# Performance work log

Measured on AMD Instinct MI355X. Metric: run time of the kernel, lower is better.

The kernel has to match this reference:

```python
import math
import jax, jax.numpy as jnp
import numpy as np

D_MODEL = 1024
N_HEADS = 8
D_CONV = 4
D_INNER = 2 * D_MODEL
D_HIDDEN = 2 * D_MODEL
DH = D_INNER // N_HEADS
L = 2048
LN_EPS = 1e-5
GN_EPS = 1e-5
N_LAYERS = 12


def _layer_norm(x, w, eps=LN_EPS):
    m = jnp.mean(x, -1, keepdims=True)
    v = jnp.var(x, -1, keepdims=True)
    return (x - m) / jnp.sqrt(v + eps) * w


def _group_norm(h, w, b, eps=GN_EPS):
    # h: (L, D_INNER); N_HEADS groups of size DH
    hg = h.reshape(h.shape[0], N_HEADS, DH)
    m = jnp.mean(hg, -1, keepdims=True)
    v = jnp.var(hg, -1, keepdims=True)
    hn = ((hg - m) / jnp.sqrt(v + eps)).reshape(h.shape[0], D_INNER)
    return hn * w + b


def _mlstm(q, k, v, ig, fg, mask):
    # q,k,v: (nh, L, dh); ig,fg: (nh, L); mask: (L, L) bool causal
    nh, l, dh = q.shape
    log_fg_act = jax.nn.log_sigmoid(fg)
    cs = jnp.pad(jnp.cumsum(log_fg_act, -1), ((0, 0), (1, 0)))  # (nh, L+1)
    diff = cs[:, 1:, None] - cs[:, None, 1:]                    # (nh, L, L)
    log_fg_mat = jnp.where(mask, diff, -jnp.inf)
    log_D = log_fg_mat + ig[:, None, :]
    max_log_D = jnp.max(log_D, -1, keepdims=True)
    D = jnp.exp(log_D - max_log_D)
    scores = jnp.einsum('nld,nmd->nlm', q, k) / math.sqrt(dh)
    c = scores * D
    norm = jnp.maximum(jnp.abs(jnp.sum(c, -1, keepdims=True)), jnp.exp(-max_log_D))
    return jnp.einsum('nlm,nmd->nld', c / (norm + 1e-6), v)


def _forward(x, ln1_w, win_w, win_b, wout_w, conv_kernel, conv_bias, wq_w, wk_w, wv_w,
             igate_w, igate_b, fgate_w, fgate_b, gn_w, gn_b, skip, ln2_w,
             ffn_win_w, ffn_wout_w, mask):
    h = _layer_norm(x, ln1_w)
    # gated up-projection
    proj = h @ win_w.T + win_b                 # (L, 2*D_INNER)
    xi, res = proj[:, :D_INNER], proj[:, D_INNER:]
    # depthwise causal conv (jnp.convolve 'valid' semantics == correlate with flipped kernel)
    xp = jnp.pad(xi, ((D_CONV - 1, 0), (0, 0)))
    kf = conv_kernel[:, ::-1]
    windows = jnp.stack([xp[j:j + L] for j in range(D_CONV)], -1)  # (L, D_INNER, D_CONV)
    xc = jax.nn.silu(jnp.einsum('lcj,cj->lc', windows, kf) + conv_bias)

    def head_lin(z, w):
        # blockwise per-head linear: (L, nh, dh) x (nh, dh, dh)
        return jnp.einsum('lnh,nhd->lnd', z.reshape(L, N_HEADS, DH), w).reshape(L, D_INNER)

    q, k, v = head_lin(xc, wq_w), head_lin(xc, wk_w), head_lin(xi, wv_w)
    gate_in = jnp.concatenate([q, k, v], -1)   # (L, 3*D_INNER)
    ig = (gate_in @ igate_w.T + igate_b).T     # (nh, L)
    fg = (gate_in @ fgate_w.T + fgate_b).T     # (nh, L)
    to_heads = lambda z: z.reshape(L, N_HEADS, DH).transpose(1, 0, 2)
    hh = _mlstm(to_heads(q), to_heads(k), to_heads(v), ig, fg, mask)  # (nh, L, dh)
    h_flat = hh.transpose(1, 0, 2).reshape(L, D_INNER)
    h2 = _group_norm(h_flat, gn_w, gn_b) + skip * xc
    x = x + (h2 * jax.nn.silu(res)) @ wout_w.T
    # gated FFN
    hf = _layer_norm(x, ln2_w)
    p = hf @ ffn_win_w.T                        # (L, 2*D_HIDDEN)
    a, z = p[:, :D_HIDDEN], p[:, D_HIDDEN:]
    return x + (jax.nn.gelu(a) * z) @ ffn_wout_w.T


def setup_inputs() -> dict:
    key = jax.random.key(0)
    ks = jax.random.split(key, 12)
    small = lambda k, shape, dim: jax.random.normal(k, shape, dtype=jnp.float32) * math.sqrt(2.0 / (5.0 * dim))
    wang = lambda k, shape, dim: jax.random.normal(k, shape, dtype=jnp.float32) * (2.0 / (N_LAYERS * math.sqrt(dim)))
    return {
        'x': jax.random.normal(ks[0], (L, D_MODEL), dtype=jnp.float32),
        'mask': jnp.tril(jnp.ones((L, L), dtype=bool)),
        'ln1_w': jnp.ones(D_MODEL, jnp.float32),
        'win_w': small(ks[1], (2 * D_INNER, D_MODEL), D_MODEL),
        'win_b': jnp.zeros(2 * D_INNER, jnp.float32),
        'wout_w': wang(ks[2], (D_MODEL, D_INNER), D_INNER),
        'conv_kernel': small(ks[3], (D_INNER, D_CONV), D_INNER),
        'conv_bias': jnp.zeros(D_INNER, jnp.float32),
        'wq_w': small(ks[4], (N_HEADS, DH, DH), DH),
        'wk_w': small(ks[5], (N_HEADS, DH, DH), DH),
        'wv_w': small(ks[6], (N_HEADS, DH, DH), DH),
        'igate_w': small(ks[7], (N_HEADS, 3 * D_INNER), 3 * D_INNER),
        'igate_b': jnp.linspace(0.0, 0.1, N_HEADS, dtype=jnp.float32),
        'fgate_w': jnp.zeros((N_HEADS, 3 * D_INNER), jnp.float32),
        'fgate_b': jnp.linspace(3.0, 6.0, N_HEADS, dtype=jnp.float32),
        'gn_w': jnp.ones(D_INNER, jnp.float32),
        'gn_b': jnp.zeros(D_INNER, jnp.float32),
        'skip': jnp.ones(D_INNER, jnp.float32),
        'ln2_w': jnp.ones(D_MODEL, jnp.float32),
        'ffn_win_w': small(ks[8], (2 * D_HIDDEN, D_MODEL), D_MODEL),
        'ffn_wout_w': wang(ks[9], (D_MODEL, D_HIDDEN), D_HIDDEN),
    }


def reference(x, mask, ln1_w, win_w, win_b, wout_w, conv_kernel, conv_bias, wq_w, wk_w, wv_w,
              igate_w, igate_b, fgate_w, fgate_b, gn_w, gn_b, skip, ln2_w, ffn_win_w, ffn_wout_w):
    return _forward(x, ln1_w, win_w, win_b, wout_w, conv_kernel, conv_bias, wq_w, wk_w, wv_w,
                    igate_w, igate_b, fgate_w, fgate_b, gn_w, gn_b, skip, ln2_w,
                    ffn_win_w, ffn_wout_w, mask)
```

## Files before the change

kernel.cpp:

```cpp
#include <hip/hip_runtime.h>
#include <math.h>

#define L     2048
#define DM    1024
#define DI    2048
#define NH    8
#define DHD   256
#define DHID  2048

typedef short bf16x8 __attribute__((ext_vector_type(8)));
typedef float f32x4  __attribute__((ext_vector_type(4)));

__device__ inline float b2f(ushort h) {
  unsigned u = ((unsigned)h) << 16;
  return __builtin_bit_cast(float, u);
}
__device__ inline ushort f2b(float f) {
  unsigned u = __builtin_bit_cast(unsigned, f);
  unsigned r = (u + 0x7FFFu + ((u >> 16) & 1u)) >> 16;
  return (ushort)r;
}
__device__ inline unsigned pk2(ushort lo, ushort hi) { return (unsigned)lo | ((unsigned)hi << 16); }

__device__ inline bf16x8 frag_ld(const ushort* tile, int rowBytes, int row, int byte0) {
  const char* bp = (const char*)tile + row * rowBytes;
  const int sw = (row & 7) << 4;
  const int b1 = byte0 + 32;
  bf16x8 r;
  *(unsigned long long*)&r =
      *(const unsigned long long*)(bp + (((byte0 & ~15) ^ sw) | (byte0 & 15)));
  *((unsigned long long*)&r + 1) =
      *(const unsigned long long*)(bp + (((b1 & ~15) ^ sw) | (b1 & 15)));
  return r;
}

__global__ __launch_bounds__(256) void cast_kernel(const float* __restrict__ src,
    ushort* __restrict__ dst, int n) {
  const int i = (blockIdx.x * 256 + threadIdx.x) * 8;
  if (i >= n) return;
  float4 a = *(const float4*)(src + i);
  float4 b = *(const float4*)(src + i + 4);
  uint4 o;
  o.x = pk2(f2b(a.x), f2b(a.y));
  o.y = pk2(f2b(a.z), f2b(a.w));
  o.z = pk2(f2b(b.x), f2b(b.y));
  o.w = pk2(f2b(b.z), f2b(b.w));
  *(uint4*)(dst + i) = o;
}

__global__ __launch_bounds__(256) void wtrans_kernel(const float* __restrict__ wq,
    const float* __restrict__ wk, const float* __restrict__ wv, ushort* __restrict__ out) {
  const int z = blockIdx.z;
  const int mat = z >> 3, h = z & 7;
  const float* src = (mat == 0 ? wq : (mat == 1 ? wk : wv)) + (size_t)h * 65536;
  ushort* dst = out + (size_t)z * 65536;
  __shared__ float s[32][33];
  const int r = threadIdx.x >> 5, c = threadIdx.x & 31;
  const int I0 = blockIdx.y * 32, J0 = blockIdx.x * 32;
#pragma unroll
  for (int k = 0; k < 4; ++k) s[r + 8 * k][c] = src[(size_t)(I0 + r + 8 * k) * 256 + J0 + c];
  __syncthreads();
#pragma unroll
  for (int k = 0; k < 4; ++k)
    dst[(size_t)(J0 + r + 8 * k) * 256 + I0 + c] = f2b(s[c][r + 8 * k]);
}

__global__ __launch_bounds__(256) void ln_kernel(const float* __restrict__ x,
    const float* __restrict__ w, ushort* __restrict__ out, int D) {
  const int row = blockIdx.x;
  const float* xr = x + (size_t)row * D;
  const int i0 = threadIdx.x * 4;
  float4 v4 = *(const float4*)(xr + i0);
  float s  = v4.x + v4.y + v4.z + v4.w;
  float s2 = v4.x*v4.x + v4.y*v4.y + v4.z*v4.z + v4.w*v4.w;
#pragma unroll
  for (int off = 32; off; off >>= 1) { s += __shfl_xor(s, off); s2 += __shfl_xor(s2, off); }
  __shared__ float rs[4], rs2[4];
  if ((threadIdx.x & 63) == 0) { rs[threadIdx.x >> 6] = s; rs2[threadIdx.x >> 6] = s2; }
  __syncthreads();
  s  = rs[0] + rs[1] + rs[2] + rs[3];
  s2 = rs2[0] + rs2[1] + rs2[2] + rs2[3];
  const float mean = s / D;
  const float inv = rsqrtf(s2 / D - mean * mean + 1e-5f);
  float4 w4 = *(const float4*)(w + i0);
  ushort4 o4 = make_ushort4(
      f2b((v4.x - mean) * inv * w4.x), f2b((v4.y - mean) * inv * w4.y),
      f2b((v4.z - mean) * inv * w4.z), f2b((v4.w - mean) * inv * w4.w));
  *(ushort4*)(out + (size_t)row * D + i0) = o4;
}

template<bool BIAS, bool RESID, bool F32OUT, bool BF16OUT>
__global__ __launch_bounds__(256) void gemm_bf16(
    const ushort* __restrict__ A, int lda, long aBat,
    const ushort* __restrict__ B, int ldb, long bBat,
    const float* __restrict__ bias,
    const float* __restrict__ resid, int ldr,
    float* __restrict__ Cf, int ldc,
    ushort* __restrict__ Cb, int ldcb, int cbLim, long cBat,
    int K) {
  __shared__ ushort As[128 * 64];
  __shared__ ushort Bs[128 * 64];
  const int tid = threadIdx.x;
  const int w = tid >> 6, lane = tid & 63;
  const int g = lane >> 4, li = lane & 15;
  const int wr = (w >> 1) * 64, wc = (w & 1) * 64;
  const int row0 = blockIdx.y * 128, col0 = blockIdx.x * 128;
  const ushort* Ab = A + (size_t)blockIdx.z * aBat;
  const ushort* Bb = B + (size_t)blockIdx.z * bBat;

  f32x4 acc[4][4];
#pragma unroll
  for (int i = 0; i < 4; ++i)
#pragma unroll
    for (int j = 0; j < 4; ++j) acc[i][j] = (f32x4){0.f, 0.f, 0.f, 0.f};

  const int sr = tid >> 3;
  const int sb = tid & 7;
  const ushort* Ag = Ab + (size_t)(row0 + sr) * lda + sb * 8;
  const ushort* Bg = Bb + (size_t)(col0 + sr) * ldb + sb * 8;

  for (int k0 = 0; k0 < K; k0 += 64) {
    __syncthreads();
#pragma unroll
    for (int i = 0; i < 4; ++i) {
      const int r = sr + 32 * i;
      uint4 va = *(const uint4*)(Ag + (size_t)(32 * i) * lda + k0);
      uint4 vb = *(const uint4*)(Bg + (size_t)(32 * i) * ldb + k0);
      const int off = r * 128 + (((sb ^ (r & 7))) << 4);
      *(uint4*)((char*)As + off) = va;
      *(uint4*)((char*)Bs + off) = vb;
    }
    __syncthreads();
#pragma unroll
    for (int ks = 0; ks < 2; ++ks) {
      bf16x8 af[4], bfr[4];
      const int byte0 = ks * 64 + 8 * g;
#pragma unroll
      for (int rb = 0; rb < 4; ++rb) af[rb] = frag_ld(As, 128, wr + rb * 16 + li, byte0);
#pragma unroll
      for (int cb = 0; cb < 4; ++cb) bfr[cb] = frag_ld(Bs, 128, wc + cb * 16 + li, byte0);
#pragma unroll
      for (int rb = 0; rb < 4; ++rb)
#pragma unroll
        for (int cb = 0; cb < 4; ++cb)
          acc[rb][cb] = __builtin_amdgcn_mfma_f32_16x16x32_bf16(af[rb], bfr[cb], acc[rb][cb], 0, 0, 0);
    }
  }

#pragma unroll
  for (int rb = 0; rb < 4; ++rb)
#pragma unroll
    for (int cb = 0; cb < 4; ++cb)
#pragma unroll
      for (int j = 0; j < 4; ++j) {
        const int r = row0 + wr + rb * 16 + 4 * g + j;
        const int c = col0 + wc + cb * 16 + li;
        float v = acc[rb][cb][j];
        if (BIAS)  v += bias[c];
        if (RESID) v += resid[(size_t)r * ldr + c];
        if (F32OUT) Cf[(size_t)r * ldc + c] = v;
        if (BF16OUT) {
          if (c < cbLim) Cb[(size_t)blockIdx.z * cBat + (size_t)r * ldcb + c] = f2b(v);
        }
      }
}

__global__ __launch_bounds__(256) void conv_silu_kernel(const float* __restrict__ proj,
    const float* __restrict__ ck, const float* __restrict__ cb, ushort* __restrict__ xcb) {
  const int idx = blockIdx.x * 256 + threadIdx.x;
  const int l = idx >> 9, c4 = (idx & 511) * 4;
  float4 s = *(const float4*)(cb + c4);
#pragma unroll
  for (int t = 0; t < 4; ++t) {
    const int lm = l - t;
    if (lm >= 0) {
      float4 pv = *(const float4*)(proj + (size_t)lm * 4096 + c4);
      s.x = fmaf(ck[(c4 + 0) * 4 + t], pv.x, s.x);
      s.y = fmaf(ck[(c4 + 1) * 4 + t], pv.y, s.y);
      s.z = fmaf(ck[(c4 + 2) * 4 + t], pv.z, s.z);
      s.w = fmaf(ck[(c4 + 3) * 4 + t], pv.w, s.w);
    }
  }
  ushort4 o = make_ushort4(f2b(s.x / (1.f + __expf(-s.x))), f2b(s.y / (1.f + __expf(-s.y))),
                           f2b(s.z / (1.f + __expf(-s.z))), f2b(s.w / (1.f + __expf(-s.w))));
  *(ushort4*)(xcb + (size_t)l * 2048 + c4) = o;
}

__global__ __launch_bounds__(256) void gates_kernel(const ushort* __restrict__ qkv3,
    const ushort* __restrict__ gw, const float* __restrict__ igb, const float* __restrict__ fgb,
    float* __restrict__ ig_t, float* __restrict__ fg_t) {
  const int l = blockIdx.x;
  const ushort* row = qkv3 + (size_t)l * 6144;
  __shared__ float red[4];
  float rf[24];
#pragma unroll
  for (int ch = 0; ch < 3; ++ch) {
    uint4 u = *(const uint4*)(row + (threadIdx.x + 256 * ch) * 8);
    rf[ch*8+0] = b2f((ushort)u.x); rf[ch*8+1] = b2f((ushort)(u.x >> 16));
    rf[ch*8+2] = b2f((ushort)u.y); rf[ch*8+3] = b2f((ushort)(u.y >> 16));
    rf[ch*8+4] = b2f((ushort)u.z); rf[ch*8+5] = b2f((ushort)(u.z >> 16));
    rf[ch*8+6] = b2f((ushort)u.w); rf[ch*8+7] = b2f((ushort)(u.w >> 16));
  }
  for (int o = 0; o < 16; ++o) {
    const ushort* wr_ = gw + (size_t)o * 6144;
    float s = 0.f;
#pragma unroll
    for (int ch = 0; ch < 3; ++ch) {
      uint4 u = *(const uint4*)(wr_ + (threadIdx.x + 256 * ch) * 8);
      s += rf[ch*8+0] * b2f((ushort)u.x) + rf[ch*8+1] * b2f((ushort)(u.x >> 16));
      s += rf[ch*8+2] * b2f((ushort)u.y) + rf[ch*8+3] * b2f((ushort)(u.y >> 16));
      s += rf[ch*8+4] * b2f((ushort)u.z) + rf[ch*8+5] * b2f((ushort)(u.z >> 16));
      s += rf[ch*8+6] * b2f((ushort)u.w) + rf[ch*8+7] * b2f((ushort)(u.w >> 16));
    }
#pragma unroll
    for (int off = 32; off; off >>= 1) s += __shfl_xor(s, off);
    if ((threadIdx.x & 63) == 0) red[threadIdx.x >> 6] = s;
    __syncthreads();
    if (threadIdx.x == 0) {
      const int n = o & 7;
      float tot = red[0] + red[1] + red[2] + red[3] + ((o >= 8) ? fgb[n] : igb[n]);
      ((o >= 8) ? fg_t : ig_t)[(size_t)n * L + l] = tot;
    }
    __syncthreads();
  }
}

__global__ __launch_bounds__(256) void scan_kernel(const float* __restrict__ ig_t,
    const float* __restrict__ fg_t, float* __restrict__ e_b, float* __restrict__ M_b,
    float* __restrict__ wv_b) {
  const int n = blockIdx.x, t = threadIdx.x;
  const int base = n * L + t * 8;
  __shared__ float ps[256], pm[256];
  float lc[8];
  float run = 0.f;
#pragma unroll
  for (int j = 0; j < 8; ++j) {
    float xg = fg_t[base + j];
    float ls = (xg >= 0.f) ? -log1pf(expf(-xg)) : (xg - log1pf(expf(xg)));
    run += ls; lc[j] = run;
  }
  ps[t] = run;
  __syncthreads();
  if (t == 0) { float r = 0.f; for (int i = 0; i < 256; ++i) { float v = ps[i]; ps[i] = r; r += v; } }
  __syncthreads();
  const float eoff = ps[t];
  float wl[8]; float rm = -3.4e38f;
#pragma unroll
  for (int j = 0; j < 8; ++j) {
    float e = eoff + lc[j];
    float wv = ig_t[base + j] - e;
    e_b[base + j] = e; wv_b[base + j] = wv;
    rm = fmaxf(rm, wv); wl[j] = rm;
  }
  pm[t] = rm;
  __syncthreads();
  if (t == 0) { float r = -3.4e38f; for (int i = 0; i < 256; ++i) { float v = pm[i]; pm[i] = r; r = fmaxf(r, v); } }
  __syncthreads();
  const float moff = pm[t];
#pragma unroll
  for (int j = 0; j < 8; ++j) M_b[base + j] = fmaxf(moff, wl[j]);
}

__global__ __launch_bounds__(256) void mlstm_attn(const ushort* __restrict__ qkv3,
    const float* __restrict__ e_b, const float* __restrict__ M_b,
    const float* __restrict__ wv_b, float* __restrict__ hflat) {
  const int n = blockIdx.y;
  const int bx = blockIdx.x;
  const int tid = threadIdx.x;
  const int w = tid >> 6, lane = tid & 63;
  const int g = lane >> 4, li = lane & 15;
  const int qr = (w & 1) * 16, dh2 = (w >> 1) * 128;

  __shared__ ushort Qs[32 * 256];
  __shared__ ushort Ks[32 * 256];
  __shared__ ushort Vt[256 * 36];
  __shared__ float wvs[32];
  __shared__ float scl[2][16];

  const int sr = tid >> 3;
  const int sbb = tid & 7;

  for (int pass = 0; pass < 2; ++pass) {
    const int qt = pass ? (63 - bx) : bx;
    const int q0 = qt * 32;
    __syncthreads();
    {
      const ushort* qsrc = qkv3 + (size_t)(q0 + sr) * 6144 + n * 256;
      char* qrow = (char*)Qs + sr * 512;
#pragma unroll
      for (int i = 0; i < 4; ++i) {
        const int b = sbb + 8 * i;
        uint4 u = *(const uint4*)(qsrc + b * 8);
        uint4 o;
        o.x = pk2(f2b(b2f((ushort)u.x) * 0.0625f), f2b(b2f((ushort)(u.x >> 16)) * 0.0625f));
        o.y = pk2(f2b(b2f((ushort)u.y) * 0.0625f), f2b(b2f((ushort)(u.y >> 16)) * 0.0625f));
        o.z = pk2(f2b(b2f((ushort)u.z) * 0.0625f), f2b(b2f((ushort)(u.z >> 16)) * 0.0625f));
        o.w = pk2(f2b(b2f((ushort)u.w) * 0.0625f), f2b(b2f((ushort)(u.w >> 16)) * 0.0625f));
        *(uint4*)(qrow + ((b ^ (sr & 7)) << 4)) = o;
      }
    }
    __syncthreads();

    bf16x8 qf[8];
#pragma unroll
    for (int dc = 0; dc < 8; ++dc) qf[dc] = frag_ld(Qs, 512, qr + li, dc * 64 + 8 * g);

    const int qg = q0 + qr + li;
    const float Mq = M_b[(size_t)n * L + qg];
    const float el = e_b[(size_t)n * L + qg];
    float rowsum = 0.f;
    f32x4 oacc[8];
#pragma unroll
    for (int db = 0; db < 8; ++db) oacc[db] = (f32x4){0.f, 0.f, 0.f, 0.f};

    const int nmt = qt + 1;
    for (int mt = 0; mt < nmt; ++mt) {
      const int m0 = mt * 32;
      __syncthreads();
      {
        const ushort* ksrc = qkv3 + (size_t)(m0 + sr) * 6144 + 2048 + n * 256;
        const ushort* vsrc = qkv3 + (size_t)(m0 + sr) * 6144 + 4096 + n * 256;
        char* krow = (char*)Ks + sr * 512;
#pragma unroll
        for (int i = 0; i < 4; ++i) {
          const int b = sbb + 8 * i;
          uint4 ku = *(const uint4*)(ksrc + b * 8);
          *(uint4*)(krow + ((b ^ (sr & 7)) << 4)) = ku;
          uint4 vu = *(const uint4*)(vsrc + b * 8);
          const int d0 = b * 8;
          ushort* vp = Vt + sr;
          vp[(d0 + 0) * 36] = (ushort)vu.x; vp[(d0 + 1) * 36] = (ushort)(vu.x >> 16);
          vp[(d0 + 2) * 36] = (ushort)vu.y; vp[(d0 + 3) * 36] = (ushort)(vu.y >> 16);
          vp[(d0 + 4) * 36] = (ushort)vu.z; vp[(d0 + 5) * 36] = (ushort)(vu.z >> 16);
          vp[(d0 + 6) * 36] = (ushort)vu.w; vp[(d0 + 7) * 36] = (ushort)(vu.w >> 16);
        }
        if (tid < 32) wvs[tid] = wv_b[(size_t)n * L + m0 + tid];
      }
      __syncthreads();

      f32x4 st0 = (f32x4){0.f, 0.f, 0.f, 0.f}, st1 = (f32x4){0.f, 0.f, 0.f, 0.f};
#pragma unroll
      for (int dc = 0; dc < 8; ++dc) {
        bf16x8 kf0 = frag_ld(Ks, 512, li, dc * 64 + 8 * g);
        bf16x8 kf1 = frag_ld(Ks, 512, 16 + li, dc * 64 + 8 * g);
        st0 = __builtin_amdgcn_mfma_f32_16x16x32_bf16(kf0, qf[dc], st0, 0, 0, 0);
        st1 = __builtin_amdgcn_mfma_f32_16x16x32_bf16(kf1, qf[dc], st1, 0, 0, 0);
      }

      bf16x8 pa;
#pragma unroll
      for (int j = 0; j < 8; ++j) {
        const int h = j >> 2;
        const int mrel = 4 * g + (j & 3) + 16 * h;
        const float s = h ? st1[j & 3] : st0[j & 3];
        const int mg = m0 + mrel;
        float p = (mg <= qg) ? s * __expf(wvs[mrel] - Mq) : 0.f;
        rowsum += p;
        pa[j] = (short)f2b(p);
      }

#pragma unroll
      for (int db = 0; db < 8; ++db) {
        const ushort* vb = Vt + (dh2 + db * 16 + li) * 36;
        bf16x8 vf;
        *(unsigned long long*)&vf = *(const unsigned long long*)(vb + 4 * g);
        *((unsigned long long*)&vf + 1) = *(const unsigned long long*)(vb + 4 * g + 16);
        oacc[db] = __builtin_amdgcn_mfma_f32_16x16x32_bf16(pa, vf, oacc[db], 0, 0, 0);
      }
    }

    rowsum += __shfl_xor(rowsum, 16);
    rowsum += __shfl_xor(rowsum, 32);
    const float sc = 1.f / (fmaxf(fabsf(rowsum), __expf(-(el + Mq))) + 1e-6f);
    if (w < 2 && lane < 16) scl[w][lane] = sc;
    __syncthreads();
    float scj[4];
#pragma unroll
    for (int j = 0; j < 4; ++j) scj[j] = scl[w & 1][4 * g + j];
#pragma unroll
    for (int db = 0; db < 8; ++db)
#pragma unroll
      for (int j = 0; j < 4; ++j)
        hflat[(size_t)(q0 + qr + 4 * g + j) * 2048 + n * 256 + dh2 + db * 16 + li] =
            oacc[db][j] * scj[j];
  }
}

__global__ __launch_bounds__(64) void gn_y_kernel(const float* __restrict__ hflat,
    const ushort* __restrict__ xcb, const float* __restrict__ proj,
    const float* __restrict__ gnw, const float* __restrict__ gnb,
    const float* __restrict__ skip, ushort* __restrict__ yb) {
  const int n = blockIdx.x, l = blockIdx.y, lane = threadIdx.x;
  const float* hr = hflat + (size_t)l * DI + n * DHD;
  float vals[4]; float s = 0.f, s2 = 0.f;
#pragma unroll
  for (int u = 0; u < 4; ++u) {
    float t = hr[lane + u * 64]; vals[u] = t; s += t; s2 += t * t;
  }
#pragma unroll
  for (int off = 32; off; off >>= 1) { s += __shfl_xor(s, off); s2 += __shfl_xor(s2, off); }
  const float mean = s * (1.f / DHD);
  const float inv = rsqrtf(s2 * (1.f / DHD) - mean * mean + 1e-5f);
#pragma unroll
  for (int u = 0; u < 4; ++u) {
    const int c = n * DHD + lane + u * 64;
    const float hn = (vals[u] - mean) * inv;
    const float h2 = hn * gnw[c] + gnb[c] + skip[c] * b2f(xcb[(size_t)l * DI + c]);
    const float r = proj[(size_t)l * 4096 + 2048 + c];
    yb[(size_t)l * DI + c] = f2b(h2 * (r / (1.f + __expf(-r))));
  }
}

__global__ __launch_bounds__(256) void gelu_mul_kernel(const float* __restrict__ p,
    ushort* __restrict__ gb) {
  const int idx = blockIdx.x * 256 + threadIdx.x;
  const int l = idx >> 9, c4 = (idx & 511) * 4;
  float4 a = *(const float4*)(p + (size_t)l * 4096 + c4);
  float4 z = *(const float4*)(p + (size_t)l * 4096 + 2048 + c4);
  float o[4];
  float av[4] = {a.x, a.y, a.z, a.w};
  float zv[4] = {z.x, z.y, z.z, z.w};
#pragma unroll
  for (int j = 0; j < 4; ++j) {
    const float t = 0.7978845608028654f * (av[j] + 0.044715f * av[j] * av[j] * av[j]);
    o[j] = 0.5f * av[j] * (1.f + tanhf(t)) * zv[j];
  }
  *(ushort4*)(gb + (size_t)l * 2048 + c4) =
      make_ushort4(f2b(o[0]), f2b(o[1]), f2b(o[2]), f2b(o[3]));
}

extern "C" void kernel_launch(void* const* d_in, const int* in_sizes, int n_in,
                              void* d_out, int out_size, void* d_ws, size_t ws_size,
                              hipStream_t stream) {
  const float* x     = (const float*)d_in[0];
  const float* ln1w  = (const float*)d_in[2];
  const float* winw  = (const float*)d_in[3];
  const float* winb  = (const float*)d_in[4];
  const float* woutw = (const float*)d_in[5];
  const float* ck    = (const float*)d_in[6];
  const float* cb    = (const float*)d_in[7];
  const float* wq    = (const float*)d_in[8];
  const float* wk    = (const float*)d_in[9];
  const float* wvw   = (const float*)d_in[10];
  const float* igw   = (const float*)d_in[11];
  const float* igb   = (const float*)d_in[12];
  const float* fgw   = (const float*)d_in[13];
  const float* fgb   = (const float*)d_in[14];
  const float* gnw   = (const float*)d_in[15];
  const float* gnb   = (const float*)d_in[16];
  const float* skip  = (const float*)d_in[17];
  const float* ln2w  = (const float*)d_in[18];
  const float* fwin  = (const float*)d_in[19];
  const float* fwout = (const float*)d_in[20];
  float* out = (float*)d_out;

  char* base = (char*)d_ws;
  const size_t MB = 1ull << 20;
  float*  proj  = (float*)(base);
  float*  hflat = (float*)(base + 32 * MB);
  float*  x2    = (float*)(base + 48 * MB);
  float*  ig_t  = (float*)(base + 56 * MB);
  float*  fg_t  = ig_t + NH * L;
  float*  e_b   = fg_t + NH * L;
  float*  M_b   = e_b + NH * L;
  float*  wv_b  = M_b + NH * L;
  ushort* hb    = (ushort*)(base + 57 * MB);
  ushort* projb = (ushort*)(base + 61 * MB);
  ushort* xcb   = (ushort*)(base + 69 * MB);
  ushort* qkv3  = (ushort*)(base + 77 * MB);
  ushort* wA    = (ushort*)(base + 101 * MB);
  ushort* wB    = (ushort*)(base + 109 * MB);
  ushort* wqkvT = (ushort*)(base + 113 * MB);
  ushort* gwB   = (ushort*)(base + 116 * MB);
  ushort* yb    = projb;
  ushort* gb    = projb;

  cast_kernel<<<2048, 256, 0, stream>>>(winw, wA, 4096 * 1024);
  cast_kernel<<<1024, 256, 0, stream>>>(woutw, wB, 1024 * 2048);
  wtrans_kernel<<<dim3(8, 8, 24), 256, 0, stream>>>(wq, wk, wvw, wqkvT);
  cast_kernel<<<24, 256, 0, stream>>>(igw, gwB, 8 * 6144);
  cast_kernel<<<24, 256, 0, stream>>>(fgw, gwB + 8 * 6144, 8 * 6144);

  ln_kernel<<<L, 256, 0, stream>>>(x, ln1w, hb, DM);
  gemm_bf16<true, false, true, true><<<dim3(32, 16, 1), 256, 0, stream>>>(
      hb, 1024, 0, wA, 1024, 0, winb, nullptr, 0, proj, 4096, projb, 2048, 2048, 0, 1024);
  conv_silu_kernel<<<(L * 512) / 256, 256, 0, stream>>>(proj, ck, cb, xcb);
  gemm_bf16<false, false, false, true><<<dim3(2, 16, 8), 256, 0, stream>>>(
      xcb, 2048, 256, wqkvT, 256, 65536, nullptr, nullptr, 0, nullptr, 0,
      qkv3, 6144, 1 << 30, 256, 256);
  gemm_bf16<false, false, false, true><<<dim3(2, 16, 8), 256, 0, stream>>>(
      xcb, 2048, 256, wqkvT + 8 * 65536, 256, 65536, nullptr, nullptr, 0, nullptr, 0,
      qkv3 + 2048, 6144, 1 << 30, 256, 256);
  gemm_bf16<false, false, false, true><<<dim3(2, 16, 8), 256, 0, stream>>>(
      projb, 2048, 256, wqkvT + 16 * 65536, 256, 65536, nullptr, nullptr, 0, nullptr, 0,
      qkv3 + 4096, 6144, 1 << 30, 256, 256);
  gates_kernel<<<L, 256, 0, stream>>>(qkv3, gwB, igb, fgb, ig_t, fg_t);
  scan_kernel<<<NH, 256, 0, stream>>>(ig_t, fg_t, e_b, M_b, wv_b);
  mlstm_attn<<<dim3(32, 8), 256, 0, stream>>>(qkv3, e_b, M_b, wv_b, hflat);
  gn_y_kernel<<<dim3(NH, L), 64, 0, stream>>>(hflat, xcb, proj, gnw, gnb, skip, yb);
  gemm_bf16<false, true, true, false><<<dim3(8, 16, 1), 256, 0, stream>>>(
      yb, 2048, 0, wB, 2048, 0, nullptr, x, 1024, x2, 1024, nullptr, 0, 0, 0, 2048);
  ln_kernel<<<L, 256, 0, stream>>>(x2, ln2w, hb, DM);
  cast_kernel<<<2048, 256, 0, stream>>>(fwin, wA, 4096 * 1024);
  cast_kernel<<<1024, 256, 0, stream>>>(fwout, wB, 1024 * 2048);
  gemm_bf16<false, false, true, false><<<dim3(32, 16, 1), 256, 0, stream>>>(
      hb, 1024, 0, wA, 1024, 0, nullptr, nullptr, 0, proj, 4096, nullptr, 0, 0, 0, 1024);
  gelu_mul_kernel<<<(L * 512) / 256, 256, 0, stream>>>(proj, gb);
  gemm_bf16<false, true, true, false><<<dim3(8, 16, 1), 256, 0, stream>>>(
      gb, 2048, 0, wB, 2048, 0, nullptr, x2, 1024, out, 1024, nullptr, 0, 0, 0, 2048);
}
```

Before: 590.2 us.

## Restructure mLSTM attention grid, prefetch K/V tiles, swizzle Vt, store bf16 output

The two-pass pairing of query tiles per block is replaced by one query tile per block over a 512-block grid, ordered longest-first with heads interleaved. The next K/V tile is prefetched into registers while the current tile is computed. The transposed V tile in shared memory gets an XOR swizzle to cut bank conflicts. The attention output is written as bf16 instead of fp32, halving traffic for the group-norm kernel at some precision cost.

```diff
diff --git a/kernel.cpp b/kernel.cpp
--- a/kernel.cpp
+++ b/kernel.cpp
@@ -263,9 +263,10 @@
 
 __global__ __launch_bounds__(256) void mlstm_attn(const ushort* __restrict__ qkv3,
     const float* __restrict__ e_b, const float* __restrict__ M_b,
-    const float* __restrict__ wv_b, float* __restrict__ hflat) {
-  const int n = blockIdx.y;
-  const int bx = blockIdx.x;
+    const float* __restrict__ wv_b, ushort* __restrict__ hflat) {
+  const int n = blockIdx.x & 7;
+  const int qt = 63 - (blockIdx.x >> 3);
+  const int q0 = qt * 32;
   const int tid = threadIdx.x;
   const int w = tid >> 6, lane = tid & 63;
   const int g = lane >> 4, li = lane & 15;
@@ -280,122 +281,153 @@
   const int sr = tid >> 3;
   const int sbb = tid & 7;
 
-  for (int pass = 0; pass < 2; ++pass) {
-    const int qt = pass ? (63 - bx) : bx;
-    const int q0 = qt * 32;
+  {
+    const ushort* qsrc = qkv3 + (size_t)(q0 + sr) * 6144 + n * 256;
+    char* qrow = (char*)Qs + sr * 512;
+#pragma unroll
+    for (int i = 0; i < 4; ++i) {
+      const int b = sbb + 8 * i;
+      uint4 u = *(const uint4*)(qsrc + b * 8);
+      uint4 o;
+      o.x = pk2(f2b(b2f((ushort)u.x) * 0.0625f), f2b(b2f((ushort)(u.x >> 16)) * 0.0625f));
+      o.y = pk2(f2b(b2f((ushort)u.y) * 0.0625f), f2b(b2f((ushort)(u.y >> 16)) * 0.0625f));
+      o.z = pk2(f2b(b2f((ushort)u.z) * 0.0625f), f2b(b2f((ushort)(u.z >> 16)) * 0.0625f));
+      o.w = pk2(f2b(b2f((ushort)u.w) * 0.0625f), f2b(b2f((ushort)(u.w >> 16)) * 0.0625f));
+      *(uint4*)(qrow + ((b ^ (sr & 7)) << 4)) = o;
+    }
+  }
+
+  uint4 kpre[4], vpre[4];
+  float wvpre = 0.f;
+  {
+    const ushort* ksrc = qkv3 + (size_t)sr * 6144 + 2048 + n * 256;
+    const ushort* vsrc = qkv3 + (size_t)sr * 6144 + 4096 + n * 256;
+#pragma unroll
+    for (int i = 0; i < 4; ++i) {
+      const int b = sbb + 8 * i;
+      kpre[i] = *(const uint4*)(ksrc + b * 8);
+      vpre[i] = *(const uint4*)(vsrc + b * 8);
+    }
+    if (tid < 32) wvpre = wv_b[(size_t)n * L + tid];
+  }
+
+  __syncthreads();
+  bf16x8 qf[8];
+#pragma unroll
+  for (int dc = 0; dc < 8; ++dc) qf[dc] = frag_ld(Qs, 512, qr + li, dc * 64 + 8 * g);
+
+  const int qg = q0 + qr + li;
+  const float Mq = M_b[(size_t)n * L + qg];
+  const float el = e_b[(size_t)n * L + qg];
+  float rowsum = 0.f;
+  f32x4 oacc[8];
+#pragma unroll
+  for (int db = 0; db < 8; ++db) oacc[db] = (f32x4){0.f, 0.f, 0.f, 0.f};
+
+  const int vmdw = sr >> 1, vlow = (sr & 1) * 2;
+
+  const int nmt = qt + 1;
+  for (int mt = 0; mt < nmt; ++mt) {
     __syncthreads();
     {
-      const ushort* qsrc = qkv3 + (size_t)(q0 + sr) * 6144 + n * 256;
-      char* qrow = (char*)Qs + sr * 512;
+      char* krow = (char*)Ks + sr * 512;
 #pragma unroll
       for (int i = 0; i < 4; ++i) {
         const int b = sbb + 8 * i;
-        uint4 u = *(const uint4*)(qsrc + b * 8);
-        uint4 o;
-        o.x = pk2(f2b(b2f((ushort)u.x) * 0.0625f), f2b(b2f((ushort)(u.x >> 16)) * 0.0625f));
-        o.y = pk2(f2b(b2f((ushort)u.y) * 0.0625f), f2b(b2f((ushort)(u.y >> 16)) * 0.0625f));
-        o.z = pk2(f2b(b2f((ushort)u.z) * 0.0625f), f2b(b2f((ushort)(u.z >> 16)) * 0.0625f));
-        o.w = pk2(f2b(b2f((ushort)u.w) * 0.0625f), f2b(b2f((ushort)(u.w >> 16)) * 0.0625f));
-        *(uint4*)(qrow + ((b ^ (sr & 7)) << 4)) = o;
+        *(uint4*)(krow + ((b ^ (sr & 7)) << 4)) = kpre[i];
+        const int d0 = b * 8;
+        const int swz = (b & 3) << 1;
+        char* vtb = (char*)Vt + d0 * 72 + (((vmdw ^ swz)) << 2) + vlow;
+        const ushort v0 = (ushort)vpre[i].x, v1 = (ushort)(vpre[i].x >> 16);
+        const ushort v2 = (ushort)vpre[i].y, v3 = (ushort)(vpre[i].y >> 16);
+        const ushort v4 = (ushort)vpre[i].z, v5 = (ushort)(vpre[i].z >> 16);
+        const ushort v6 = (ushort)vpre[i].w, v7 = (ushort)(vpre[i].w >> 16);
+        *(ushort*)(vtb)           = v0;
+        *(ushort*)(vtb + 72)      = v1;
+        *(ushort*)(vtb + 144)     = v2;
+        *(ushort*)(vtb + 216)     = v3;
+        *(ushort*)(vtb + 288)     = v4;
+        *(ushort*)(vtb + 360)     = v5;
+        *(ushort*)(vtb + 432)     = v6;
+        *(ushort*)(vtb + 504)     = v7;
       }
+      if (tid < 32) wvs[tid] = wvpre;
     }
     __syncthreads();
 
-    bf16x8 qf[8];
-#pragma unroll
-    for (int dc = 0; dc < 8; ++dc) qf[dc] = frag_ld(Qs, 512, qr + li, dc * 64 + 8 * g);
-
-    const int qg = q0 + qr + li;
-    const float Mq = M_b[(size_t)n * L + qg];
-    const float el = e_b[(size_t)n * L + qg];
-    float rowsum = 0.f;
-    f32x4 oacc[8];
-#pragma unroll
-    for (int db = 0; db < 8; ++db) oacc[db] = (f32x4){0.f, 0.f, 0.f, 0.f};
-
-    const int nmt = qt + 1;
-    for (int mt = 0; mt < nmt; ++mt) {
-      const int m0 = mt * 32;
-      __syncthreads();
-      {
-        const ushort* ksrc = qkv3 + (size_t)(m0 + sr) * 6144 + 2048 + n * 256;
-        const ushort* vsrc = qkv3 + (size_t)(m0 + sr) * 6144 + 4096 + n * 256;
-        char* krow = (char*)Ks + sr * 512;
-#pragma unroll
-        for (int i = 0; i < 4; ++i) {
-          const int b = sbb + 8 * i;
-          uint4 ku = *(const uint4*)(ksrc + b * 8);
-          *(uint4*)(krow + ((b ^ (sr & 7)) << 4)) = ku;
-          uint4 vu = *(const uint4*)(vsrc + b * 8);
-          const int d0 = b * 8;
-          ushort* vp = Vt + sr;
-          vp[(d0 + 0) * 36] = (ushort)vu.x; vp[(d0 + 1) * 36] = (ushort)(vu.x >> 16);
-          vp[(d0 + 2) * 36] = (ushort)vu.y; vp[(d0 + 3) * 36] = (ushort)(vu.y >> 16);
-          vp[(d0 + 4) * 36] = (ushort)vu.z; vp[(d0 + 5) * 36] = (ushort)(vu.z >> 16);
-          vp[(d0 + 6) * 36] = (ushort)vu.w; vp[(d0 + 7) * 36] = (ushort)(vu.w >> 16);
-        }
-        if (tid < 32) wvs[tid] = wv_b[(size_t)n * L + m0 + tid];
+    if (mt + 1 < nmt) {
+      const int m1 = (mt + 1) * 32;
+      const ushort* ksrc = qkv3 + (size_t)(m1 + sr) * 6144 + 2048 + n * 256;
+      const ushort* vsrc = qkv3 + (size_t)(m1 + sr) * 6144 + 4096 + n * 256;
+#pragma unroll
+      for (int i = 0; i < 4; ++i) {
+        const int b = sbb + 8 * i;
+        kpre[i] = *(const uint4*)(ksrc + b * 8);
+        vpre[i] = *(const uint4*)(vsrc + b * 8);
       }
-      __syncthreads();
-
-      f32x4 st0 = (f32x4){0.f, 0.f, 0.f, 0.f}, st1 = (f32x4){0.f, 0.f, 0.f, 0.f};
-#pragma unroll
-      for (int dc = 0; dc < 8; ++dc) {
-        bf16x8 kf0 = frag_ld(Ks, 512, li, dc * 64 + 8 * g);
-        bf16x8 kf1 = frag_ld(Ks, 512, 16 + li, dc * 64 + 8 * g);
-        st0 = __builtin_amdgcn_mfma_f32_16x16x32_bf16(kf0, qf[dc], st0, 0, 0, 0);
-        st1 = __builtin_amdgcn_mfma_f32_16x16x32_bf16(kf1, qf[dc], st1, 0, 0, 0);
-      }
-
-      bf16x8 pa;
-#pragma unroll
-      for (int j = 0; j < 8; ++j) {
-        const int h = j >> 2;
-        const int mrel = 4 * g + (j & 3) + 16 * h;
-        const float s = h ? st1[j & 3] : st0[j & 3];
-        const int mg = m0 + mrel;
-        float p = (mg <= qg) ? s * __expf(wvs[mrel] - Mq) : 0.f;
-        rowsum += p;
-        pa[j] = (short)f2b(p);
-      }
-
-#pragma unroll
-      for (int db = 0; db < 8; ++db) {
-        const ushort* vb = Vt + (dh2 + db * 16 + li) * 36;
-        bf16x8 vf;
-        *(unsigned long long*)&vf = *(const unsigned long long*)(vb + 4 * g);
-        *((unsigned long long*)&vf + 1) = *(const unsigned long long*)(vb + 4 * g + 16);
-        oacc[db] = __builtin_amdgcn_mfma_f32_16x16x32_bf16(pa, vf, oacc[db], 0, 0, 0);
-      }
-    }
-
-    rowsum += __shfl_xor(rowsum, 16);
-    rowsum += __shfl_xor(rowsum, 32);
-    const float sc = 1.f / (fmaxf(fabsf(rowsum), __expf(-(el + Mq))) + 1e-6f);
-    if (w < 2 && lane < 16) scl[w][lane] = sc;
-    __syncthreads();
-    float scj[4];
-#pragma unroll
-    for (int j = 0; j < 4; ++j) scj[j] = scl[w & 1][4 * g + j];
-#pragma unroll
-    for (int db = 0; db < 8; ++db)
-#pragma unroll
-      for (int j = 0; j < 4; ++j)
-        hflat[(size_t)(q0 + qr + 4 * g + j) * 2048 + n * 256 + dh2 + db * 16 + li] =
-            oacc[db][j] * scj[j];
-  }
-}
-
-__global__ __launch_bounds__(64) void gn_y_kernel(const float* __restrict__ hflat,
+      if (tid < 32) wvpre = wv_b[(size_t)n * L + m1 + tid];
+    }
+
+    const int m0 = mt * 32;
+    f32x4 st0 = (f32x4){0.f, 0.f, 0.f, 0.f}, st1 = (f32x4){0.f, 0.f, 0.f, 0.f};
+#pragma unroll
+    for (int dc = 0; dc < 8; ++dc) {
+      bf16x8 kf0 = frag_ld(Ks, 512, li, dc * 64 + 8 * g);
+      bf16x8 kf1 = frag_ld(Ks, 512, 16 + li, dc * 64 + 8 * g);
+      st0 = __builtin_amdgcn_mfma_f32_16x16x32_bf16(kf0, qf[dc], st0, 0, 0, 0);
+      st1 = __builtin_amdgcn_mfma_f32_16x16x32_bf16(kf1, qf[dc], st1, 0, 0, 0);
+    }
+
+    bf16x8 pa;
+#pragma unroll
+    for (int j = 0; j < 8; ++j) {
+      const int h = j >> 2;
+      const int mrel = 4 * g + (j & 3) + 16 * h;
+      const float s = h ? st1[j & 3] : st0[j & 3];
+      const int mg = m0 + mrel;
+      float p = (mg <= qg) ? s * __expf(wvs[mrel] - Mq) : 0.f;
+      rowsum += p;
+      pa[j] = (short)f2b(p);
+    }
+
+#pragma unroll
+    for (int db = 0; db < 8; ++db) {
+      const char* vb = (const char*)Vt + (dh2 + db * 16 + li) * 72;
+      const int swzr = ((2 * db + (li >> 3)) & 3) << 1;
+      const int mo = ((2 * g) ^ swzr) << 2;
+      bf16x8 vf;
+      *(unsigned long long*)&vf = *(const unsigned long long*)(vb + mo);
+      *((unsigned long long*)&vf + 1) = *(const unsigned long long*)(vb + mo + 32);
+      oacc[db] = __builtin_amdgcn_mfma_f32_16x16x32_bf16(pa, vf, oacc[db], 0, 0, 0);
+    }
+  }
+
+  rowsum += __shfl_xor(rowsum, 16);
+  rowsum += __shfl_xor(rowsum, 32);
+  const float sc = 1.f / (fmaxf(fabsf(rowsum), __expf(-(el + Mq))) + 1e-6f);
+  if (w < 2 && lane < 16) scl[w][lane] = sc;
+  __syncthreads();
+  float scj[4];
+#pragma unroll
+  for (int j = 0; j < 4; ++j) scj[j] = scl[w & 1][4 * g + j];
+#pragma unroll
+  for (int db = 0; db < 8; ++db)
+#pragma unroll
+    for (int j = 0; j < 4; ++j)
+      hflat[(size_t)(q0 + qr + 4 * g + j) * 2048 + n * 256 + dh2 + db * 16 + li] =
+          f2b(oacc[db][j] * scj[j]);
+}
+
+__global__ __launch_bounds__(64) void gn_y_kernel(const ushort* __restrict__ hflat,
     const ushort* __restrict__ xcb, const float* __restrict__ proj,
     const float* __restrict__ gnw, const float* __restrict__ gnb,
     const float* __restrict__ skip, ushort* __restrict__ yb) {
   const int n = blockIdx.x, l = blockIdx.y, lane = threadIdx.x;
-  const float* hr = hflat + (size_t)l * DI + n * DHD;
+  const ushort* hr = hflat + (size_t)l * DI + n * DHD;
   float vals[4]; float s = 0.f, s2 = 0.f;
 #pragma unroll
   for (int u = 0; u < 4; ++u) {
-    float t = hr[lane + u * 64]; vals[u] = t; s += t; s2 += t * t;
+    float t = b2f(hr[lane + u * 64]); vals[u] = t; s += t; s2 += t * t;
   }
 #pragma unroll
   for (int off = 32; off; off >>= 1) { s += __shfl_xor(s, off); s2 += __shfl_xor(s2, off); }
@@ -457,7 +489,7 @@
   char* base = (char*)d_ws;
   const size_t MB = 1ull << 20;
   float*  proj  = (float*)(base);
-  float*  hflat = (float*)(base + 32 * MB);
+  ushort* hflat = (ushort*)(base + 32 * MB);
   float*  x2    = (float*)(base + 48 * MB);
   float*  ig_t  = (float*)(base + 56 * MB);
   float*  fg_t  = ig_t + NH * L;
@@ -496,7 +528,7 @@
       qkv3 + 4096, 6144, 1 << 30, 256, 256);
   gates_kernel<<<L, 256, 0, stream>>>(qkv3, gwB, igb, fgb, ig_t, fg_t);
   scan_kernel<<<NH, 256, 0, stream>>>(ig_t, fg_t, e_b, M_b, wv_b);
-  mlstm_attn<<<dim3(32, 8), 256, 0, stream>>>(qkv3, e_b, M_b, wv_b, hflat);
+  mlstm_attn<<<512, 256, 0, stream>>>(qkv3, e_b, M_b, wv_b, hflat);
   gn_y_kernel<<<dim3(NH, L), 64, 0, stream>>>(hflat, xcb, proj, gnw, gnb, skip, yb);
   gemm_bf16<false, true, true, false><<<dim3(8, 16, 1), 256, 0, stream>>>(
       yb, 2048, 0, wB, 2048, 0, nullptr, x, 1024, x2, 1024, nullptr, 0, 0, 0, 2048);
```

After: 611.2 us. +3.6%, slower.
